# Kernel optimization log

Measured on AMD Instinct MI355X. Metric: run time of the kernel, lower is better.

The kernel has to match this reference:

```python
import jax, jax.numpy as jnp
import numpy as np

CENTER_DROP = 3.0  # center_drop_grid_size from __init__


def _polar_grid(Hp, Wp, Hc, Wc):
    # Reproduces the 'in'-mode grid built in Cart2Polar.__init__ (ij meshgrid),
    # returning grid_sample pixel coords (align_corners=True) and scatter indices.
    yy, xx = jnp.meshgrid(jnp.arange(Hp, dtype=jnp.float32),
                          jnp.arange(Wp, dtype=jnp.float32), indexing='ij')
    theta = np.float32(np.pi) - xx / Wp * np.float32(2.0 * np.pi)
    r = (Hp - 0.5 - yy + CENTER_DROP) / (Hp + CENTER_DROP) * (Wc / 2.0)
    index_x = r * jnp.cos(theta) + Wc / 2.0
    index_y = r * jnp.sin(theta) + Wc / 2.0
    # normalize to [-1,1] (as stored buffer), then un-normalize per grid_sample
    nx = index_x / Wc * 2.0 - 1.0
    ny = index_y / Wc * 2.0 - 1.0
    gx = (nx + 1.0) * 0.5 * (Wc - 1)  # x coord samples width dim
    gy = (ny + 1.0) * 0.5 * (Hc - 1)  # y coord samples height dim
    yi = yy.reshape(-1).astype(jnp.int32)
    xi = xx.reshape(-1).astype(jnp.int32)
    return gx.reshape(-1), gy.reshape(-1), yi, xi


def _bilinear_sample(img, gx, gy):
    # img [B,C,H,W]; gx,gy [B,N] pixel coords; bilinear, zeros padding, align_corners=True
    H, W = img.shape[2], img.shape[3]
    x0 = jnp.floor(gx)
    y0 = jnp.floor(gy)
    wx1 = gx - x0
    wy1 = gy - y0
    x1 = x0 + 1.0
    y1 = y0 + 1.0

    def gather(ix, iy):
        valid = ((ix >= 0) & (ix < W) & (iy >= 0) & (iy < H)).astype(img.dtype)
        ixc = jnp.clip(ix, 0, W - 1).astype(jnp.int32)
        iyc = jnp.clip(iy, 0, H - 1).astype(jnp.int32)
        vals = jax.vmap(lambda im, yid, xid: im[:, yid, xid])(img, iyc, ixc)  # [B,C,N]
        return vals * valid[:, None, :]

    return (gather(x0, y0) * ((1.0 - wx1) * (1.0 - wy1))[:, None, :]
            + gather(x1, y0) * (wx1 * (1.0 - wy1))[:, None, :]
            + gather(x0, y1) * ((1.0 - wx1) * wy1)[:, None, :]
            + gather(x1, y1) * (wx1 * wy1)[:, None, :])


def setup_inputs() -> dict:
    key = jax.random.key(0)
    k1, k2 = jax.random.split(key)
    grid_feat = jax.random.normal(k1, (4, 64, 480, 480), dtype=jnp.float32)
    ref_feat = jax.random.normal(k2, (4, 64, 480, 360), dtype=jnp.float32)
    return {"grid_feat": grid_feat, "ref_feat": ref_feat}


def reference(grid_feat, ref_feat):
    B, C, Hc, Wc = grid_feat.shape
    Hp, Wp = ref_feat.shape[2], ref_feat.shape[3]
    gx, gy, yi, xi = _polar_grid(Hp, Wp, Hc, Wc)  # [N], N = Hp*Wp
    N = gx.shape[0]
    gxb = jnp.broadcast_to(gx, (B, N))
    gyb = jnp.broadcast_to(gy, (B, N))
    sampled = _bilinear_sample(grid_feat, gxb, gyb)          # [B,C,N]
    sampled = sampled.transpose(0, 2, 1)                     # [B,N,C]
    # scatter into polar layout: polar_feat[b, :, y, x] = sampled row
    out = ref_feat.transpose(0, 2, 3, 1)                     # [B,Hp,Wp,C]
    out = out.at[:, yi, xi].set(sampled)
    return out.transpose(0, 3, 1, 2)                         # [B,C,Hp,Wp]
```

## Files before the change

### kernel.cpp

```cpp
#include <hip/hip_runtime.h>
#include <hip/hip_bf16.h>
#include <math.h>


#define BB 4
#define CC 64
#define HC 480
#define WC 480
#define HP 480
#define WP 360

#define TY 16
#define TX 16
#define BYT (HP / TY)
#define BXT ((WP + TX - 1) / TX)
#define CSPLIT 2
#define CCB (CC / CSPLIT)
#define NWG (BB * BYT * BXT * CSPLIT)
#define CB 16

typedef float f2a __attribute__((ext_vector_type(2), aligned(4)));

__global__ __launch_bounds__(256) void c2p_kernel(const float* __restrict__ g,
                                                  float* __restrict__ out) {
    __shared__ float lds[CB][TY][TX + 1];

    const int logical = blockIdx.x;
    const int h  = logical & (CSPLIT - 1);
    const int t1 = logical >> 1;
    const int xt = t1 % BXT;
    const int t2 = t1 / BXT;
    const int yt = t2 % BYT;
    const int b  = t2 / BYT;

    const int tid  = threadIdx.x;
    const int lane = tid & 63;
    const int w    = tid >> 6;
    const int ly = lane >> 2;
    const int lx = (w << 2) | (lane & 3);
    const int y  = yt * TY + ly;
    const int x  = xt * TX + lx;

    const float PI = 3.14159265358979323846f;
    float theta = PI - (float)x * (2.0f * PI / (float)WP);
    float r = ((float)HP - 0.5f - (float)y + 3.0f) * (1.0f / ((float)HP + 3.0f)) * ((float)WC * 0.5f);
    float s, c;
    __sincosf(theta, &s, &c);
    float index_x = r * c + (float)WC * 0.5f;
    float index_y = r * s + (float)WC * 0.5f;
    const float scale = (float)(WC - 1) / (float)WC;
    float gx = index_x * scale;
    float gy = index_y * scale;

    float x0f = floorf(gx);
    float y0f = floorf(gy);
    float wx1 = gx - x0f;
    float wy1 = gy - y0f;
    float wx0 = 1.0f - wx1;
    float wy0 = 1.0f - wy1;

    const int x0 = (int)x0f;
    const int y0 = (int)y0f;

    const float w00 = wx0 * wy0;
    const float w10 = wx1 * wy0;
    const float w01 = wx0 * wy1;
    const float w11 = wx1 * wy1;

    const int o0 = y0 * WC + x0;
    const int o1 = o0 + WC;

    constexpr int HWc = HC * WC;
    constexpr int HWp = HP * WP;

    const float* __restrict__ base = g + ((size_t)b * CC + h * CCB) * HWc;

    const int srow = tid >> 4;
    const int scol = tid & 15;
    const int sy = yt * TY + srow;
    const int sx = xt * TX + scol;
    const bool sok = (sx < WP);
    float* __restrict__ ob = out + ((size_t)b * CC + h * CCB) * HWp + (size_t)sy * WP + sx;

    f2a a0[CB], a1[CB];

#pragma unroll
    for (int j = 0; j < CB; ++j) {
        const float* __restrict__ p = base + (size_t)j * HWc;
        a0[j] = *(const f2a*)(p + o0);
        a1[j] = *(const f2a*)(p + o1);
    }
    __builtin_amdgcn_sched_barrier(0);

#pragma unroll
    for (int cb = 0; cb < CCB; cb += CB) {
        float v[CB];
#pragma unroll
        for (int j = 0; j < CB; ++j)
            v[j] = a0[j].x * w00 + a0[j].y * w10 + a1[j].x * w01 + a1[j].y * w11;

        __syncthreads();
#pragma unroll
        for (int j = 0; j < CB; ++j)
            lds[j][ly][lx] = v[j];
        __syncthreads();

        if (cb + CB < CCB) {
#pragma unroll
            for (int j = 0; j < CB; ++j) {
                const float* __restrict__ p = base + (size_t)(cb + CB + j) * HWc;
                a0[j] = *(const f2a*)(p + o0);
                a1[j] = *(const f2a*)(p + o1);
            }
            __builtin_amdgcn_sched_barrier(0);
        }

        if (sok) {
#pragma unroll
            for (int j = 0; j < CB; ++j)
                __builtin_nontemporal_store(lds[j][srow][scol], &ob[(size_t)(cb + j) * HWp]);
        }
    }
}

extern "C" void kernel_launch(void* const* d_in, const int* in_sizes, int n_in,
                              void* d_out, int out_size, void* d_ws, size_t ws_size,
                              hipStream_t stream) {
    const float* grid_feat = (const float*)d_in[0];
    float* out = (float*)d_out;
    c2p_kernel<<<NWG, 256, 0, stream>>>(grid_feat, out);
}
```

Baseline: 144.2 us.

## Stage per-tile source window in LDS and sample bilinear taps from shared memory

Each workgroup now covers a 32x8 output tile. It computes the bounding box of its source taps with a wave-shuffle and LDS reduction, then cooperatively loads a 40x40 window per channel into double-buffered LDS with coalesced dword loads. The four bilinear taps are read from LDS instead of as per-thread scattered global pair loads, and results are stored directly without the LDS transpose. The goal is fewer redundant, uncoalesced gathers. The risk is a sync per channel, serialized loads with a full vmcnt wait, and a 40x40 window that may not cover every tile's footprint near the polar center, which would give wrong results.

After: 291.1 us. +101.8%, slower.

```diff
diff --git a/kernel.cpp b/kernel.cpp
--- a/kernel.cpp
+++ b/kernel.cpp
@@ -10,20 +10,24 @@
 #define HP 480
 #define WP 360
 
-#define TY 16
-#define TX 16
+#define TY 32
+#define TX 8
 #define BYT (HP / TY)
-#define BXT ((WP + TX - 1) / TX)
+#define BXT (WP / TX)
 #define CSPLIT 2
 #define CCB (CC / CSPLIT)
 #define NWG (BB * BYT * BXT * CSPLIT)
-#define CB 16
 
-typedef float f2a __attribute__((ext_vector_type(2), aligned(4)));
+#define WIN 40
+#define WSTR 41
+#define NSLOT (WIN * WSTR)
+#define LDSZ (NSLOT + 1)
+#define NIT 7
 
-__global__ __launch_bounds__(256) void c2p_kernel(const float* __restrict__ g,
-                                                  float* __restrict__ out) {
-    __shared__ float lds[CB][TY][TX + 1];
+__global__ __launch_bounds__(256, 4) void c2p_kernel(const float* __restrict__ g,
+                                                     float* __restrict__ out) {
+    __shared__ float sbuf[2][LDSZ];
+    __shared__ int red[2][4];
 
     const int logical = blockIdx.x;
     const int h  = logical & (CSPLIT - 1);
@@ -36,18 +40,18 @@
     const int tid  = threadIdx.x;
     const int lane = tid & 63;
     const int w    = tid >> 6;
-    const int ly = lane >> 2;
-    const int lx = (w << 2) | (lane & 3);
-    const int y  = yt * TY + ly;
-    const int x  = xt * TX + lx;
+    const int orow = tid >> 3;
+    const int ocol = tid & 7;
+    const int y = yt * TY + orow;
+    const int x = xt * TX + ocol;
 
     const float PI = 3.14159265358979323846f;
     float theta = PI - (float)x * (2.0f * PI / (float)WP);
     float r = ((float)HP - 0.5f - (float)y + 3.0f) * (1.0f / ((float)HP + 3.0f)) * ((float)WC * 0.5f);
-    float s, c;
-    __sincosf(theta, &s, &c);
-    float index_x = r * c + (float)WC * 0.5f;
-    float index_y = r * s + (float)WC * 0.5f;
+    float sn, cs;
+    __sincosf(theta, &sn, &cs);
+    float index_x = r * cs + (float)WC * 0.5f;
+    float index_y = r * sn + (float)WC * 0.5f;
     const float scale = (float)(WC - 1) / (float)WC;
     float gx = index_x * scale;
     float gy = index_y * scale;
@@ -67,60 +71,81 @@
     const float w01 = wx0 * wy1;
     const float w11 = wx1 * wy1;
 
-    const int o0 = y0 * WC + x0;
-    const int o1 = o0 + WC;
+    int lo_y = y0, lo_x = x0;
+#pragma unroll
+    for (int off = 32; off; off >>= 1) {
+        lo_y = min(lo_y, __shfl_xor(lo_y, off));
+        lo_x = min(lo_x, __shfl_xor(lo_x, off));
+    }
+    if (lane == 0) { red[0][w] = lo_y; red[1][w] = lo_x; }
+    __syncthreads();
+    const int ymin = min(min(red[0][0], red[0][1]), min(red[0][2], red[0][3]));
+    const int xmin = min(min(red[1][0], red[1][1]), min(red[1][2], red[1][3]));
+
+    int voff[NIT], loff[NIT];
+#pragma unroll
+    for (int k = 0; k < NIT; ++k) {
+        const int idx = tid + 256 * k;
+        const int row = (idx * 1639) >> 16;
+        const int col = idx - row * 40;
+        const int gyc = min(ymin + row, HC - 1);
+        const int gxc = min(xmin + col, WC - 1);
+        voff[k] = (gyc * WC + gxc) * 4;
+        loff[k] = (idx < WIN * WIN) ? (idx + row) : NSLOT;
+    }
 
     constexpr int HWc = HC * WC;
     constexpr int HWp = HP * WP;
+    const float* __restrict__ base = g + ((size_t)b * CC + (size_t)h * CCB) * HWc;
+    float* __restrict__ ob = out + ((size_t)b * CC + (size_t)h * CCB) * HWp
+                                 + (size_t)y * WP + x;
+    const int sidx = (y0 - ymin) * WSTR + (x0 - xmin);
 
-    const float* __restrict__ base = g + ((size_t)b * CC + h * CCB) * HWc;
+    float v[CCB];
+    float st[NIT];
 
-    const int srow = tid >> 4;
-    const int scol = tid & 15;
-    const int sy = yt * TY + srow;
-    const int sx = xt * TX + scol;
-    const bool sok = (sx < WP);
-    float* __restrict__ ob = out + ((size_t)b * CC + h * CCB) * HWp + (size_t)sy * WP + sx;
-
-    f2a a0[CB], a1[CB];
+    {
+        const float* gch = base;
+#pragma unroll
+        for (int k = 0; k < NIT; ++k)
+            asm volatile("global_load_dword %0, %1, %2"
+                         : "=v"(st[k]) : "v"(voff[k]), "s"(gch));
+        asm volatile("s_waitcnt vmcnt(0)" ::: "memory");
+        __builtin_amdgcn_sched_barrier(0);
+#pragma unroll
+        for (int k = 0; k < NIT; ++k) sbuf[0][loff[k]] = st[k];
+        __syncthreads();
+    }
 
 #pragma unroll
-    for (int j = 0; j < CB; ++j) {
-        const float* __restrict__ p = base + (size_t)j * HWc;
-        a0[j] = *(const f2a*)(p + o0);
-        a1[j] = *(const f2a*)(p + o1);
+    for (int j = 0; j < CCB; ++j) {
+        const int p = j & 1;
+        if (j + 1 < CCB) {
+            const float* gch = base + (size_t)(j + 1) * HWc;
+#pragma unroll
+            for (int k = 0; k < NIT; ++k)
+                asm volatile("global_load_dword %0, %1, %2"
+                             : "=v"(st[k]) : "v"(voff[k]), "s"(gch));
+        }
+        const float* __restrict__ sb = sbuf[p];
+        const float s00 = sb[sidx];
+        const float s10 = sb[sidx + 1];
+        const float s01 = sb[sidx + WSTR];
+        const float s11 = sb[sidx + WSTR + 1];
+        v[j] = s00 * w00 + s10 * w10 + s01 * w01 + s11 * w11;
+
+        if (j + 1 < CCB) {
+            asm volatile("s_waitcnt vmcnt(0)" ::: "memory");
+            __builtin_amdgcn_sched_barrier(0);
+#pragma unroll
+            for (int k = 0; k < NIT; ++k) sbuf[p ^ 1][loff[k]] = st[k];
+        }
+        __syncthreads();
     }
-    __builtin_amdgcn_sched_barrier(0);
 
 #pragma unroll
-    for (int cb = 0; cb < CCB; cb += CB) {
-        float v[CB];
-#pragma unroll
-        for (int j = 0; j < CB; ++j)
-            v[j] = a0[j].x * w00 + a0[j].y * w10 + a1[j].x * w01 + a1[j].y * w11;
-
-        __syncthreads();
-#pragma unroll
-        for (int j = 0; j < CB; ++j)
-            lds[j][ly][lx] = v[j];
-        __syncthreads();
-
-        if (cb + CB < CCB) {
-#pragma unroll
-            for (int j = 0; j < CB; ++j) {
-                const float* __restrict__ p = base + (size_t)(cb + CB + j) * HWc;
-                a0[j] = *(const f2a*)(p + o0);
-                a1[j] = *(const f2a*)(p + o1);
-            }
-            __builtin_amdgcn_sched_barrier(0);
-        }
-
-        if (sok) {
-#pragma unroll
-            for (int j = 0; j < CB; ++j)
-                __builtin_nontemporal_store(lds[j][srow][scol], &ob[(size_t)(cb + j) * HWp]);
-        }
-    }
+    for (int j = 0; j < CCB; ++j)
+        __builtin_nontemporal_store(v[j], &ob[(size_t)j * HWp]);
 }
 
 extern "C" void kernel_launch(void* const* d_in, const int* in_sizes, int n_in,
```
